# Kernel tuning notes

Measured on AMD Instinct MI355X. Metric: run time of the kernel, lower is better.

The kernel has to match this reference:

```python
import jax, jax.numpy as jnp
import numpy as np
from jax import lax

EPS = 1e-8
CAGE_SIZE = 1.4
DIST_THRESH = 0.4
CAGE_ITERS = 100
CAGE_STEP = 0.01


def _icosphere_div1():
    # icosahedron with one loop subdivision -> 42 verts, 80 faces, unit sphere
    t = (1.0 + 5.0 ** 0.5) / 2.0
    v = np.array([[-1, t, 0], [1, t, 0], [-1, -t, 0], [1, -t, 0],
                  [0, -1, t], [0, 1, t], [0, -1, -t], [0, 1, -t],
                  [t, 0, -1], [t, 0, 1], [-t, 0, -1], [-t, 0, 1]], dtype=np.float64)
    v /= np.linalg.norm(v, axis=1, keepdims=True)
    f = [[0, 11, 5], [0, 5, 1], [0, 1, 7], [0, 7, 10], [0, 10, 11],
         [1, 5, 9], [5, 11, 4], [11, 10, 2], [10, 7, 6], [7, 1, 8],
         [3, 9, 4], [3, 4, 2], [3, 2, 6], [3, 6, 8], [3, 8, 9],
         [4, 9, 5], [2, 4, 11], [6, 2, 10], [8, 6, 7], [9, 8, 1]]
    verts = list(v)
    cache = {}
    def mid(a, b):
        key = (min(a, b), max(a, b))
        if key not in cache:
            m = verts[a] + verts[b]
            verts.append(m / np.linalg.norm(m))
            cache[key] = len(verts) - 1
        return cache[key]
    nf = []
    for a, b, c in f:
        ab, bc, ca = mid(a, b), mid(b, c), mid(c, a)
        nf += [[a, ab, ca], [b, bc, ab], [c, ca, bc], [ab, bc, ca]]
    return np.stack(verts).astype(np.float32), np.array(nf, dtype=np.int32)


def _optimize_cage(cage, shape):
    # cage: (B,3,V), shape: (B,3,N). Pull cage toward origin until close to shape.
    def step(c, _):
        diff = c[:, :, :, None] - shape[:, :, None, :]          # (B,3,V,N)
        dist = jnp.sqrt(jnp.sum(diff * diff, axis=1))           # (B,V,N)
        min_d = jnp.min(dist, axis=2)                           # (B,V)
        upd = (min_d > DIST_THRESH).astype(c.dtype)
        return c + CAGE_STEP * (-c) * upd[:, None], None
    cage, _ = lax.scan(step, cage, None, length=CAGE_ITERS)
    return cage


def _mvc_weights(query, verts, faces):
    # 3D mean value coordinates (Ju et al. 2005).
    # query: (B,P,3), verts: (B,V,3), faces: (F,3) int -> weights (B,P,V)
    B, P, _ = query.shape
    V = verts.shape[1]
    F = faces.shape[0]
    u = verts[:, None] - query[:, :, None]                      # (B,P,V,3)
    d = jnp.linalg.norm(u, axis=-1)                             # (B,P,V)
    u = u / jnp.maximum(d, EPS)[..., None]
    uf = u[:, :, faces]                                         # (B,P,F,3,3)
    df = d[:, :, faces]                                         # (B,P,F,3)
    # edge lengths on unit sphere between opposite corner directions
    l = jnp.linalg.norm(jnp.roll(uf, -1, axis=3) - jnp.roll(uf, 1, axis=3), axis=-1)  # (B,P,F,3)
    theta = 2.0 * jnp.arcsin(jnp.clip(0.5 * l, 0.0, 1.0))
    h = 0.5 * jnp.sum(theta, axis=-1)                           # (B,P,F)
    sin_t = jnp.sin(theta)
    c = (2.0 * jnp.sin(h)[..., None] * jnp.sin(h[..., None] - theta)
         / jnp.maximum(jnp.roll(sin_t, -1, axis=-1) * jnp.roll(sin_t, 1, axis=-1), EPS)) - 1.0
    u0, u1, u2 = uf[..., 0, :], uf[..., 1, :], uf[..., 2, :]
    det = jnp.sum(u0 * jnp.cross(u1, u2), axis=-1)              # (B,P,F)
    s = jnp.sign(det)[..., None] * jnp.sqrt(jnp.clip(1.0 - c * c, 0.0, None))  # (B,P,F,3)
    valid = jnp.all(jnp.abs(s) > EPS, axis=-1)                  # coplanar-outside -> face contributes 0
    num = (theta - jnp.roll(c, -1, axis=-1) * jnp.roll(theta, 1, axis=-1)
           - jnp.roll(c, 1, axis=-1) * jnp.roll(theta, -1, axis=-1))
    den = df * jnp.roll(sin_t, -1, axis=-1) * jnp.roll(s, 1, axis=-1)
    den = jnp.where(jnp.abs(den) > EPS, den, jnp.where(den >= 0, EPS, -EPS))
    w = jnp.where(valid[..., None], num / den, 0.0)             # (B,P,F,3)
    W = jnp.zeros((B, P, V), dtype=query.dtype).at[:, :, faces.reshape(-1)].add(
        w.reshape(B, P, F * 3))
    sW = jnp.sum(W, axis=-1, keepdims=True)
    sW = jnp.where(jnp.abs(sW) > EPS, sW, EPS)
    return W / sW


def setup_inputs() -> dict:
    key = jax.random.key(0)
    ks = jax.random.split(key, 5)
    B, N, K = 4, 6144, 8
    v, f = _icosphere_div1()
    template_vertices = jnp.asarray(CAGE_SIZE * v.T[None])      # (1,3,42)
    return {
        "catModel": jax.random.normal(ks[0], (B, N, 3), dtype=jnp.float32),
        "catKeys": jax.random.normal(ks[1], (B, K, 3), dtype=jnp.float32),
        "catInflu": 0.1 * jax.random.normal(ks[2], (B, K, 42), dtype=jnp.float32),
        "insKeys": jax.random.normal(ks[3], (B, K, 3), dtype=jnp.float32),
        "insModel": jax.random.normal(ks[4], (B, N, 3), dtype=jnp.float32),
        "template_vertices": template_vertices,
        "template_faces": jnp.asarray(f),
    }


def reference(catModel, catKeys, catInflu, insKeys, insModel, template_vertices, template_faces):
    B = catModel.shape[0]
    cat_sh = jnp.swapaxes(catModel, 1, 2)                       # (B,3,N)
    cage = jnp.broadcast_to(template_vertices, (B,) + template_vertices.shape[1:])  # (B,3,42)
    cage = _optimize_cage(cage, cat_sh)
    # keypoint-driven cage offset via influence matrix
    kp_off = jnp.swapaxes(insKeys - catKeys, 1, 2)              # (B,3,8)
    cage_off = jnp.sum(kp_off[..., None] * catInflu[:, None], axis=2)  # (B,3,42)
    new_cage = cage + cage_off
    cage_v = jnp.swapaxes(cage, 1, 2)                           # (B,42,3)
    new_cage_v = jnp.swapaxes(new_cage, 1, 2)
    weights = _mvc_weights(catModel, cage_v, template_faces)    # (B,N,42)
    deformed = jnp.einsum('bnv,bvd->bnd', weights, new_cage_v)  # (B,N,3)
    # symmetric chamfer (squared L2, mean over points then batch, summed directions)
    d2 = jnp.sum((deformed[:, :, None] - insModel[:, None]) ** 2, axis=-1)  # (B,N,N)
    sim_loss = jnp.mean(jnp.min(d2, axis=2)) + jnp.mean(jnp.min(d2, axis=1))
    return (catModel, insModel, deformed, sim_loss)
```

## Files before the change

kernel.cpp:

```cpp
#include <hip/hip_runtime.h>
#include <hip/hip_bf16.h>
#include <math.h>

#define EPSF 1e-8f

static constexpr int FI[80][3] = {
  {0,12,14},{11,13,12},{5,14,13},{12,13,14},
  {0,14,16},{5,15,14},{1,16,15},{14,15,16},
  {0,16,18},{1,17,16},{7,18,17},{16,17,18},
  {0,18,20},{7,19,18},{10,20,19},{18,19,20},
  {0,20,12},{10,21,20},{11,12,21},{20,21,12},
  {1,15,23},{5,22,15},{9,23,22},{15,22,23},
  {5,13,25},{11,24,13},{4,25,24},{13,24,25},
  {11,21,27},{10,26,21},{2,27,26},{21,26,27},
  {10,19,29},{7,28,19},{6,29,28},{19,28,29},
  {7,17,31},{1,30,17},{8,31,30},{17,30,31},
  {3,32,34},{9,33,32},{4,34,33},{32,33,34},
  {3,34,36},{4,35,34},{2,36,35},{34,35,36},
  {3,36,38},{2,37,36},{6,38,37},{36,37,38},
  {3,38,40},{6,39,38},{8,40,39},{38,39,40},
  {3,40,32},{8,41,40},{9,32,41},{40,41,32},
  {4,33,25},{9,22,33},{5,25,22},{33,22,25},
  {2,35,27},{4,24,35},{11,27,24},{35,24,27},
  {6,37,29},{2,26,37},{10,29,26},{37,26,29},
  {8,39,31},{6,28,39},{7,31,28},{39,28,31},
  {9,41,23},{8,30,41},{1,23,30},{41,30,23}
};

__global__ __launch_bounds__(512) void k_cage(
    const float* __restrict__ catModel,
    const float* __restrict__ tv,
    const float* __restrict__ catKeys,
    const float* __restrict__ insKeys,
    const float* __restrict__ catInflu,
    float* __restrict__ cage,
    float* __restrict__ ncage)
{
  const int b = blockIdx.x / 42, v = blockIdx.x % 42;
  const int tid = threadIdx.x;
  const int lane = tid & 63, w = tid >> 6;
  const float c0x = tv[v], c0y = tv[42 + v], c0z = tv[84 + v];
  const float a = c0x*c0x + c0y*c0y + c0z*c0z;

  float pb2[12], pc[12];
  const float* P = catModel + (size_t)b * 6144 * 3;
  #pragma unroll
  for (int j = 0; j < 12; ++j) {
    int n = tid + j * 512;
    float px = P[n*3+0], py = P[n*3+1], pz = P[n*3+2];
    pb2[j] = -2.0f * (c0x*px + c0y*py + c0z*pz);
    pc[j]  = px*px + py*py + pz*pz;
  }

  __shared__ int mm[8];
  __shared__ float sfin;

  int tmin = 1000;
  float s = 1.0f;
  for (int t = 0; t < 100; ++t) {
    float ma = 1e30f, mb = 1e30f, mc = 1e30f, md = 1e30f;
    #pragma unroll
    for (int j = 0; j < 12; j += 4) {
      ma = fminf(ma, fmaf(fmaf(a, s, pb2[j+0]), s, pc[j+0]));
      mb = fminf(mb, fmaf(fmaf(a, s, pb2[j+1]), s, pc[j+1]));
      mc = fminf(mc, fmaf(fmaf(a, s, pb2[j+2]), s, pc[j+2]));
      md = fminf(md, fmaf(fmaf(a, s, pb2[j+3]), s, pc[j+3]));
    }
    float m = fminf(fminf(ma, mb), fminf(mc, md));
    if (m <= 0.16f && tmin == 1000) tmin = t;
    if (__all(tmin != 1000)) break;
    s *= 0.99f;
  }

  #pragma unroll
  for (int off = 32; off; off >>= 1)
    tmin = min(tmin, __shfl_xor(tmin, off, 64));
  if (lane == 0) mm[w] = tmin;
  __syncthreads();

  if (tid == 0) {
    int k = mm[0];
    #pragma unroll
    for (int i = 1; i < 8; ++i) k = min(k, mm[i]);
    if (k > 100) k = 100;
    float sf = 1.0f;
    for (int i = 0; i < k; ++i) sf *= 0.99f;
    sfin = sf;
  }
  __syncthreads();

  if (tid < 3) {
    const int d = tid;
    const float cg = sfin * tv[d*42 + v];
    float off = 0.0f;
    #pragma unroll
    for (int k = 0; k < 8; ++k)
      off += (insKeys[(b*8+k)*3 + d] - catKeys[(b*8+k)*3 + d]) * catInflu[(b*8+k)*42 + v];
    cage [(b*42 + v)*3 + d] = cg;
    ncage[(b*42 + v)*3 + d] = cg + off;
  }
}

__global__ __launch_bounds__(256) void k_mvc(
    const float* __restrict__ catModel,
    const float* __restrict__ cage,
    const float* __restrict__ ncage,
    float* __restrict__ outCat,
    float* __restrict__ outDef)
{
  const int b    = blockIdx.x / 384;
  const int pblk = blockIdx.x % 384;
  const int lane = threadIdx.x & 63;
  const int w    = threadIdx.x >> 6;
  const int pt   = lane & 15;
  const int sub  = lane >> 4;
  const int slice = w*4 + sub;
  const int p    = pblk * 16 + pt;

  __shared__ float cv[126], nv[126];
  __shared__ unsigned sF[80];
  __shared__ float red[4][4][16];
  if (threadIdx.x < 126) {
    cv[threadIdx.x] = cage [b*126 + threadIdx.x];
    nv[threadIdx.x] = ncage[b*126 + threadIdx.x];
  }
  if (threadIdx.x < 80) {
    sF[threadIdx.x] = (unsigned)FI[threadIdx.x][0]
                    | ((unsigned)FI[threadIdx.x][1] << 8)
                    | ((unsigned)FI[threadIdx.x][2] << 16);
  }
  __syncthreads();

  const float qx = catModel[((size_t)b*6144 + p)*3 + 0];
  const float qy = catModel[((size_t)b*6144 + p)*3 + 1];
  const float qz = catModel[((size_t)b*6144 + p)*3 + 2];

  if (w == 1 && sub == 0) {
    outCat[((size_t)b*6144 + p)*3 + 0] = qx;
    outCat[((size_t)b*6144 + p)*3 + 1] = qy;
    outCat[((size_t)b*6144 + p)*3 + 2] = qz;
  }

  float sW = 0.0f, dx = 0.0f, dy = 0.0f, dz = 0.0f;

  for (int ff = 0; ff < 5; ++ff) {
    const unsigned pk = sF[slice*5 + ff];
    const int i0 = pk & 255, i1 = (pk >> 8) & 255, i2 = pk >> 16;

    float e0x = cv[i0*3+0]-qx, e0y = cv[i0*3+1]-qy, e0z = cv[i0*3+2]-qz;
    float e1x = cv[i1*3+0]-qx, e1y = cv[i1*3+1]-qy, e1z = cv[i1*3+2]-qz;
    float e2x = cv[i2*3+0]-qx, e2y = cv[i2*3+1]-qy, e2z = cv[i2*3+2]-qz;
    float d0 = sqrtf(e0x*e0x + e0y*e0y + e0z*e0z);
    float d1 = sqrtf(e1x*e1x + e1y*e1y + e1z*e1z);
    float d2 = sqrtf(e2x*e2x + e2y*e2y + e2z*e2z);
    float r0 = 1.0f / fmaxf(d0, EPSF);
    float r1 = 1.0f / fmaxf(d1, EPSF);
    float r2 = 1.0f / fmaxf(d2, EPSF);
    float u0x = e0x*r0, u0y = e0y*r0, u0z = e0z*r0;
    float u1x = e1x*r1, u1y = e1y*r1, u1z = e1z*r1;
    float u2x = e2x*r2, u2y = e2y*r2, u2z = e2z*r2;

    float ax_ = u1x-u2x, ay_ = u1y-u2y, az_ = u1z-u2z;
    float bx_ = u2x-u0x, by_ = u2y-u0y, bz_ = u2z-u0z;
    float cx_ = u0x-u1x, cy_ = u0y-u1y, cz_ = u0z-u1z;
    float l0 = sqrtf(ax_*ax_ + ay_*ay_ + az_*az_);
    float l1 = sqrtf(bx_*bx_ + by_*by_ + bz_*bz_);
    float l2 = sqrtf(cx_*cx_ + cy_*cy_ + cz_*cz_);

    float s0 = fminf(0.5f*l0, 1.0f);
    float s1 = fminf(0.5f*l1, 1.0f);
    float s2 = fminf(0.5f*l2, 1.0f);
    float th0 = 2.0f*asinf(s0), th1 = 2.0f*asinf(s1), th2 = 2.0f*asinf(s2);
    float co0 = sqrtf(fmaxf(fmaf(-s0, s0, 1.0f), 0.0f));
    float co1 = sqrtf(fmaxf(fmaf(-s1, s1, 1.0f), 0.0f));
    float co2 = sqrtf(fmaxf(fmaf(-s2, s2, 1.0f), 0.0f));
    float st0 = 2.0f*s0*co0;
    float st1 = 2.0f*s1*co1;
    float st2 = 2.0f*s2*co2;

    float Sh = s0*co1*co2 + co0*s1*co2 + co0*co1*s2 - s0*s1*s2;
    float Ch = co0*co1*co2 - s0*s1*co2 - s0*co1*s2 - co0*s1*s2;
    float sh0 = Sh*fmaf(-2.0f*s0, s0, 1.0f) - Ch*st0;
    float sh1 = Sh*fmaf(-2.0f*s1, s1, 1.0f) - Ch*st1;
    float sh2 = Sh*fmaf(-2.0f*s2, s2, 1.0f) - Ch*st2;

    float c0 = 2.0f*Sh*sh0 / fmaxf(st1*st2, EPSF) - 1.0f;
    float c1 = 2.0f*Sh*sh1 / fmaxf(st2*st0, EPSF) - 1.0f;
    float c2 = 2.0f*Sh*sh2 / fmaxf(st0*st1, EPSF) - 1.0f;

    float det = u0x*(u1y*u2z - u1z*u2y)
              + u0y*(u1z*u2x - u1x*u2z)
              + u0z*(u1x*u2y - u1y*u2x);
    float sg = (det > 0.0f) ? 1.0f : ((det < 0.0f) ? -1.0f : 0.0f);
    float q0 = sg * sqrtf(fmaxf(fmaf(-c0, c0, 1.0f), 0.0f));
    float q1 = sg * sqrtf(fmaxf(fmaf(-c1, c1, 1.0f), 0.0f));
    float q2 = sg * sqrtf(fmaxf(fmaf(-c2, c2, 1.0f), 0.0f));
    bool valid = (fabsf(q0) > EPSF) && (fabsf(q1) > EPSF) && (fabsf(q2) > EPSF);

    float n0 = th0 - c1*th2 - c2*th1;
    float n1 = th1 - c2*th0 - c0*th2;
    float n2 = th2 - c0*th1 - c1*th0;
    float de0 = d0*st1*q2;
    float de1 = d1*st2*q0;
    float de2 = d2*st0*q1;
    de0 = (fabsf(de0) > EPSF) ? de0 : ((de0 >= 0.0f) ? EPSF : -EPSF);
    de1 = (fabsf(de1) > EPSF) ? de1 : ((de1 >= 0.0f) ? EPSF : -EPSF);
    de2 = (fabsf(de2) > EPSF) ? de2 : ((de2 >= 0.0f) ? EPSF : -EPSF);

    if (valid) {
      float w0 = n0/de0, w1 = n1/de1, w2 = n2/de2;
      sW += w0 + w1 + w2;
      dx = fmaf(w0, nv[i0*3+0], fmaf(w1, nv[i1*3+0], fmaf(w2, nv[i2*3+0], dx)));
      dy = fmaf(w0, nv[i0*3+1], fmaf(w1, nv[i1*3+1], fmaf(w2, nv[i2*3+1], dy)));
      dz = fmaf(w0, nv[i0*3+2], fmaf(w1, nv[i1*3+2], fmaf(w2, nv[i2*3+2], dz)));
    }
  }

  sW += __shfl_xor(sW, 16, 64); dx += __shfl_xor(dx, 16, 64);
  dy += __shfl_xor(dy, 16, 64); dz += __shfl_xor(dz, 16, 64);
  sW += __shfl_xor(sW, 32, 64); dx += __shfl_xor(dx, 32, 64);
  dy += __shfl_xor(dy, 32, 64); dz += __shfl_xor(dz, 32, 64);

  if (sub == 0) {
    red[w][0][pt] = sW; red[w][1][pt] = dx;
    red[w][2][pt] = dy; red[w][3][pt] = dz;
  }
  __syncthreads();

  if (w == 0 && sub == 0) {
    float S = red[0][0][pt] + red[1][0][pt] + red[2][0][pt] + red[3][0][pt];
    float X = red[0][1][pt] + red[1][1][pt] + red[2][1][pt] + red[3][1][pt];
    float Y = red[0][2][pt] + red[1][2][pt] + red[2][2][pt] + red[3][2][pt];
    float Z = red[0][3][pt] + red[1][3][pt] + red[2][3][pt] + red[3][3][pt];
    S = (fabsf(S) > EPSF) ? S : EPSF;
    float inv = 1.0f / S;
    outDef[((size_t)b*6144 + p)*3 + 0] = X * inv;
    outDef[((size_t)b*6144 + p)*3 + 1] = Y * inv;
    outDef[((size_t)b*6144 + p)*3 + 2] = Z * inv;
  }
}

__global__ __launch_bounds__(256) void k_chamfer(
    const float* __restrict__ def,
    const float* __restrict__ ins,
    float*       __restrict__ outIns,
    float*       __restrict__ partial,
    float*       __restrict__ loss)
{
  const int bx  = blockIdx.x;
  const int dir = (bx >= 384) ? 1 : 0;
  const int r   = bx - dir*384;
  const int b   = r / 96;
  const int rt  = (r % 96) / 24;
  const int cc  = r % 24;
  const int tid = threadIdx.x;

  if (bx == 0 && tid == 0) loss[0] = 0.0f;

  const float* R = (dir ? ins : def) + (size_t)b * 6144 * 3;
  const float* C = (dir ? def : ins) + (size_t)b * 6144 * 3;

  const int r0 = rt*1536 + tid;
  float rx[6], ry[6], rz[6];
  #pragma unroll
  for (int k = 0; k < 6; ++k) {
    int rr = r0 + k*256;
    rx[k] = R[rr*3+0]; ry[k] = R[rr*3+1]; rz[k] = R[rr*3+2];
  }

  if (dir == 1 && cc == 0) {
    #pragma unroll
    for (int k = 0; k < 6; ++k) {
      int rr = r0 + k*256;
      outIns[(size_t)(b*6144 + rr)*3+0] = rx[k];
      outIns[(size_t)(b*6144 + rr)*3+1] = ry[k];
      outIns[(size_t)(b*6144 + rr)*3+2] = rz[k];
    }
  }

  __shared__ float4 tile[256];
  {
    int c = cc*256 + tid;
    float cx = C[c*3+0], cy = C[c*3+1], cz = C[c*3+2];
    tile[tid] = make_float4(-2.0f*cx, -2.0f*cy, -2.0f*cz, cx*cx + cy*cy + cz*cz);
  }
  __syncthreads();

  float m[6];
  #pragma unroll
  for (int k = 0; k < 6; ++k) m[k] = 1e30f;

  #pragma unroll 8
  for (int j = 0; j < 256; ++j) {
    float4 q = tile[j];
    #pragma unroll
    for (int k = 0; k < 6; ++k)
      m[k] = fminf(m[k], fmaf(q.x, rx[k], fmaf(q.y, ry[k], fmaf(q.z, rz[k], q.w))));
  }

  float* po = partial + ((size_t)((dir*4 + b)*24 + cc)) * 6144;
  #pragma unroll
  for (int k = 0; k < 6; ++k) {
    int rr = r0 + k*256;
    po[rr] = m[k] + (rx[k]*rx[k] + ry[k]*ry[k] + rz[k]*rz[k]);
  }
}

__global__ __launch_bounds__(256) void k_loss(
    const float* __restrict__ partial,
    float* __restrict__ loss)
{
  const int base = blockIdx.x * 512 + threadIdx.x * 2;
  float s = 0.0f;
  #pragma unroll
  for (int g = base; g < base + 2; ++g) {
    const int db = g / 6144, row = g % 6144;
    const float* pp = partial + (size_t)db * 24 * 6144 + row;
    float v = 1e30f;
    #pragma unroll
    for (int c = 0; c < 24; ++c) v = fminf(v, pp[c * 6144]);
    s += v;
  }
  #pragma unroll
  for (int off = 32; off; off >>= 1) s += __shfl_xor(s, off, 64);
  __shared__ float red[4];
  if ((threadIdx.x & 63) == 0) red[threadIdx.x >> 6] = s;
  __syncthreads();
  if (threadIdx.x == 0)
    atomicAdd(loss, (red[0] + red[1] + red[2] + red[3]) * (1.0f / 24576.0f));
}

extern "C" void kernel_launch(void* const* d_in, const int* in_sizes, int n_in,
                              void* d_out, int out_size, void* d_ws, size_t ws_size,
                              hipStream_t stream) {
  const float* catModel = (const float*)d_in[0];
  const float* catKeys  = (const float*)d_in[1];
  const float* catInflu = (const float*)d_in[2];
  const float* insKeys  = (const float*)d_in[3];
  const float* insModel = (const float*)d_in[4];
  const float* tv       = (const float*)d_in[5];

  float* out = (float*)d_out;
  float* ws  = (float*)d_ws;
  float* cage    = ws;
  float* ncage   = ws + 512;
  float* partial = ws + 1024;

  k_cage<<<168, 512, 0, stream>>>(catModel, tv, catKeys, insKeys, catInflu, cage, ncage);
  k_mvc <<<1536, 256, 0, stream>>>(catModel, cage, ncage, out, out + 147456);
  k_chamfer<<<768, 256, 0, stream>>>(out + 147456, insModel, out + 73728, partial, out + 221184);
  k_loss<<<96, 256, 0, stream>>>(partial, out + 221184);
}
```

Measured before the change: 138.0 us.

## Fuse cage, MVC, chamfer and loss into one cooperative kernel with grid syncs

Replaces the four separate kernel launches with a single cooperative kernel of 512 blocks that runs each stage in turn, with grid.sync between stages, so launch gaps and inter-kernel drain are removed. Each block processes several MVC point tiles and up to two chamfer tiles. The cage stage now uses 256 threads per block, so each thread holds twice as many points, and only 168 of 512 blocks do work in that stage. If the cooperative launch fails, it falls back to the original four-kernel path. This adds grid-wide barrier cost, and the fused kernel's register pressure may limit occupancy.

```diff
diff --git a/kernel.cpp b/kernel.cpp
--- a/kernel.cpp
+++ b/kernel.cpp
@@ -1,6 +1,9 @@
 #include <hip/hip_runtime.h>
 #include <hip/hip_bf16.h>
+#include <hip/hip_cooperative_groups.h>
 #include <math.h>
+
+namespace cg = cooperative_groups;
 
 #define EPSF 1e-8f
 
@@ -27,122 +30,11 @@
   {9,41,23},{8,30,41},{1,23,30},{41,30,23}
 };
 
-__global__ __launch_bounds__(512) void k_cage(
-    const float* __restrict__ catModel,
-    const float* __restrict__ tv,
-    const float* __restrict__ catKeys,
-    const float* __restrict__ insKeys,
-    const float* __restrict__ catInflu,
-    float* __restrict__ cage,
-    float* __restrict__ ncage)
+__device__ __forceinline__ void mvc_slice(
+    const float* cv, const float* nv, const unsigned* sF,
+    int slice, float qx, float qy, float qz,
+    float& sW, float& dx, float& dy, float& dz)
 {
-  const int b = blockIdx.x / 42, v = blockIdx.x % 42;
-  const int tid = threadIdx.x;
-  const int lane = tid & 63, w = tid >> 6;
-  const float c0x = tv[v], c0y = tv[42 + v], c0z = tv[84 + v];
-  const float a = c0x*c0x + c0y*c0y + c0z*c0z;
-
-  float pb2[12], pc[12];
-  const float* P = catModel + (size_t)b * 6144 * 3;
-  #pragma unroll
-  for (int j = 0; j < 12; ++j) {
-    int n = tid + j * 512;
-    float px = P[n*3+0], py = P[n*3+1], pz = P[n*3+2];
-    pb2[j] = -2.0f * (c0x*px + c0y*py + c0z*pz);
-    pc[j]  = px*px + py*py + pz*pz;
-  }
-
-  __shared__ int mm[8];
-  __shared__ float sfin;
-
-  int tmin = 1000;
-  float s = 1.0f;
-  for (int t = 0; t < 100; ++t) {
-    float ma = 1e30f, mb = 1e30f, mc = 1e30f, md = 1e30f;
-    #pragma unroll
-    for (int j = 0; j < 12; j += 4) {
-      ma = fminf(ma, fmaf(fmaf(a, s, pb2[j+0]), s, pc[j+0]));
-      mb = fminf(mb, fmaf(fmaf(a, s, pb2[j+1]), s, pc[j+1]));
-      mc = fminf(mc, fmaf(fmaf(a, s, pb2[j+2]), s, pc[j+2]));
-      md = fminf(md, fmaf(fmaf(a, s, pb2[j+3]), s, pc[j+3]));
-    }
-    float m = fminf(fminf(ma, mb), fminf(mc, md));
-    if (m <= 0.16f && tmin == 1000) tmin = t;
-    if (__all(tmin != 1000)) break;
-    s *= 0.99f;
-  }
-
-  #pragma unroll
-  for (int off = 32; off; off >>= 1)
-    tmin = min(tmin, __shfl_xor(tmin, off, 64));
-  if (lane == 0) mm[w] = tmin;
-  __syncthreads();
-
-  if (tid == 0) {
-    int k = mm[0];
-    #pragma unroll
-    for (int i = 1; i < 8; ++i) k = min(k, mm[i]);
-    if (k > 100) k = 100;
-    float sf = 1.0f;
-    for (int i = 0; i < k; ++i) sf *= 0.99f;
-    sfin = sf;
-  }
-  __syncthreads();
-
-  if (tid < 3) {
-    const int d = tid;
-    const float cg = sfin * tv[d*42 + v];
-    float off = 0.0f;
-    #pragma unroll
-    for (int k = 0; k < 8; ++k)
-      off += (insKeys[(b*8+k)*3 + d] - catKeys[(b*8+k)*3 + d]) * catInflu[(b*8+k)*42 + v];
-    cage [(b*42 + v)*3 + d] = cg;
-    ncage[(b*42 + v)*3 + d] = cg + off;
-  }
-}
-
-__global__ __launch_bounds__(256) void k_mvc(
-    const float* __restrict__ catModel,
-    const float* __restrict__ cage,
-    const float* __restrict__ ncage,
-    float* __restrict__ outCat,
-    float* __restrict__ outDef)
-{
-  const int b    = blockIdx.x / 384;
-  const int pblk = blockIdx.x % 384;
-  const int lane = threadIdx.x & 63;
-  const int w    = threadIdx.x >> 6;
-  const int pt   = lane & 15;
-  const int sub  = lane >> 4;
-  const int slice = w*4 + sub;
-  const int p    = pblk * 16 + pt;
-
-  __shared__ float cv[126], nv[126];
-  __shared__ unsigned sF[80];
-  __shared__ float red[4][4][16];
-  if (threadIdx.x < 126) {
-    cv[threadIdx.x] = cage [b*126 + threadIdx.x];
-    nv[threadIdx.x] = ncage[b*126 + threadIdx.x];
-  }
-  if (threadIdx.x < 80) {
-    sF[threadIdx.x] = (unsigned)FI[threadIdx.x][0]
-                    | ((unsigned)FI[threadIdx.x][1] << 8)
-                    | ((unsigned)FI[threadIdx.x][2] << 16);
-  }
-  __syncthreads();
-
-  const float qx = catModel[((size_t)b*6144 + p)*3 + 0];
-  const float qy = catModel[((size_t)b*6144 + p)*3 + 1];
-  const float qz = catModel[((size_t)b*6144 + p)*3 + 2];
-
-  if (w == 1 && sub == 0) {
-    outCat[((size_t)b*6144 + p)*3 + 0] = qx;
-    outCat[((size_t)b*6144 + p)*3 + 1] = qy;
-    outCat[((size_t)b*6144 + p)*3 + 2] = qz;
-  }
-
-  float sW = 0.0f, dx = 0.0f, dy = 0.0f, dz = 0.0f;
-
   for (int ff = 0; ff < 5; ++ff) {
     const unsigned pk = sF[slice*5 + ff];
     const int i0 = pk & 255, i1 = (pk >> 8) & 255, i2 = pk >> 16;
@@ -215,6 +107,350 @@
       dz = fmaf(w0, nv[i0*3+2], fmaf(w1, nv[i1*3+2], fmaf(w2, nv[i2*3+2], dz)));
     }
   }
+}
+
+__global__ __launch_bounds__(256, 2) void k_fused(
+    const float* __restrict__ catModel, const float* __restrict__ catKeys,
+    const float* __restrict__ catInflu, const float* __restrict__ insKeys,
+    const float* __restrict__ insModel, const float* __restrict__ tv,
+    float* __restrict__ outCat, float* __restrict__ outIns,
+    float* __restrict__ outDef, float* __restrict__ loss,
+    float* __restrict__ cage, float* __restrict__ ncage,
+    float* __restrict__ partial)
+{
+  cg::grid_group grid = cg::this_grid();
+  const int bx  = blockIdx.x;
+  const int tid = threadIdx.x;
+  const int lane = tid & 63;
+  const int w    = tid >> 6;
+
+  __shared__ int   mm[4];
+  __shared__ float sfin;
+  __shared__ float cv[126], nv[126];
+  __shared__ unsigned sF[80];
+  __shared__ float red[4][4][16];
+  __shared__ float4 tile[256];
+  __shared__ float lred[4];
+
+  if (bx == 0 && tid == 0) loss[0] = 0.0f;
+  if (bx < 168) {
+    const int b = bx / 42, v = bx % 42;
+    const float c0x = tv[v], c0y = tv[42 + v], c0z = tv[84 + v];
+    const float a = c0x*c0x + c0y*c0y + c0z*c0z;
+
+    float pb2[24], pc[24];
+    const float* P = catModel + (size_t)b * 6144 * 3;
+    #pragma unroll
+    for (int j = 0; j < 24; ++j) {
+      int n = tid + j * 256;
+      float px = P[n*3+0], py = P[n*3+1], pz = P[n*3+2];
+      pb2[j] = -2.0f * (c0x*px + c0y*py + c0z*pz);
+      pc[j]  = px*px + py*py + pz*pz;
+    }
+
+    int tmin = 1000;
+    float s = 1.0f;
+    for (int t = 0; t < 100; ++t) {
+      float ma = 1e30f, mb = 1e30f, mc = 1e30f, md = 1e30f;
+      #pragma unroll
+      for (int j = 0; j < 24; j += 4) {
+        ma = fminf(ma, fmaf(fmaf(a, s, pb2[j+0]), s, pc[j+0]));
+        mb = fminf(mb, fmaf(fmaf(a, s, pb2[j+1]), s, pc[j+1]));
+        mc = fminf(mc, fmaf(fmaf(a, s, pb2[j+2]), s, pc[j+2]));
+        md = fminf(md, fmaf(fmaf(a, s, pb2[j+3]), s, pc[j+3]));
+      }
+      float m = fminf(fminf(ma, mb), fminf(mc, md));
+      if (m <= 0.16f && tmin == 1000) tmin = t;
+      if (__all(tmin != 1000)) break;
+      s *= 0.99f;
+    }
+
+    #pragma unroll
+    for (int off = 32; off; off >>= 1)
+      tmin = min(tmin, __shfl_xor(tmin, off, 64));
+    if (lane == 0) mm[w] = tmin;
+    __syncthreads();
+
+    if (tid == 0) {
+      int k = min(min(mm[0], mm[1]), min(mm[2], mm[3]));
+      if (k > 100) k = 100;
+      float sf = 1.0f;
+      for (int i = 0; i < k; ++i) sf *= 0.99f;
+      sfin = sf;
+    }
+    __syncthreads();
+
+    if (tid < 3) {
+      const int d = tid;
+      const float cg_ = sfin * tv[d*42 + v];
+      float off = 0.0f;
+      #pragma unroll
+      for (int k = 0; k < 8; ++k)
+        off += (insKeys[(b*8+k)*3 + d] - catKeys[(b*8+k)*3 + d]) * catInflu[(b*8+k)*42 + v];
+      cage [(b*42 + v)*3 + d] = cg_;
+      ncage[(b*42 + v)*3 + d] = cg_ + off;
+    }
+  }
+
+  __threadfence();
+  grid.sync();
+
+  {
+    const int job0 = bx * 3;
+    const int b = job0 / 384;
+    if (tid < 126) {
+      cv[tid] = cage [b*126 + tid];
+      nv[tid] = ncage[b*126 + tid];
+    }
+    if (tid < 80) {
+      sF[tid] = (unsigned)FI[tid][0] | ((unsigned)FI[tid][1] << 8)
+              | ((unsigned)FI[tid][2] << 16);
+    }
+    __syncthreads();
+
+    const int pt   = lane & 15;
+    const int sub  = lane >> 4;
+    const int slice = w*4 + sub;
+
+    for (int h = 0; h < 3; ++h) {
+      const int pblk = (job0 + h) % 384;
+      const int p    = pblk * 16 + pt;
+
+      const float qx = catModel[((size_t)b*6144 + p)*3 + 0];
+      const float qy = catModel[((size_t)b*6144 + p)*3 + 1];
+      const float qz = catModel[((size_t)b*6144 + p)*3 + 2];
+
+      if (w == 1 && sub == 0) {
+        outCat[((size_t)b*6144 + p)*3 + 0] = qx;
+        outCat[((size_t)b*6144 + p)*3 + 1] = qy;
+        outCat[((size_t)b*6144 + p)*3 + 2] = qz;
+      }
+
+      float sW = 0.0f, dx = 0.0f, dy = 0.0f, dz = 0.0f;
+      mvc_slice(cv, nv, sF, slice, qx, qy, qz, sW, dx, dy, dz);
+
+      sW += __shfl_xor(sW, 16, 64); dx += __shfl_xor(dx, 16, 64);
+      dy += __shfl_xor(dy, 16, 64); dz += __shfl_xor(dz, 16, 64);
+      sW += __shfl_xor(sW, 32, 64); dx += __shfl_xor(dx, 32, 64);
+      dy += __shfl_xor(dy, 32, 64); dz += __shfl_xor(dz, 32, 64);
+
+      if (sub == 0) {
+        red[w][0][pt] = sW; red[w][1][pt] = dx;
+        red[w][2][pt] = dy; red[w][3][pt] = dz;
+      }
+      __syncthreads();
+
+      if (w == 0 && sub == 0) {
+        float S = red[0][0][pt] + red[1][0][pt] + red[2][0][pt] + red[3][0][pt];
+        float X = red[0][1][pt] + red[1][1][pt] + red[2][1][pt] + red[3][1][pt];
+        float Y = red[0][2][pt] + red[1][2][pt] + red[2][2][pt] + red[3][2][pt];
+        float Z = red[0][3][pt] + red[1][3][pt] + red[2][3][pt] + red[3][3][pt];
+        S = (fabsf(S) > EPSF) ? S : EPSF;
+        float inv = 1.0f / S;
+        outDef[((size_t)b*6144 + p)*3 + 0] = X * inv;
+        outDef[((size_t)b*6144 + p)*3 + 1] = Y * inv;
+        outDef[((size_t)b*6144 + p)*3 + 2] = Z * inv;
+      }
+      __syncthreads();
+    }
+  }
+
+  __threadfence();
+  grid.sync();
+
+  for (int jj = 0; jj < 2; ++jj) {
+    const int jb = bx + jj*512;
+    if (jb >= 768) break;
+    const int dir = (jb >= 384) ? 1 : 0;
+    const int r   = jb - dir*384;
+    const int b   = r / 96;
+    const int rt  = (r % 96) / 24;
+    const int cc  = r % 24;
+
+    const float* R = (dir ? insModel : outDef) + (size_t)b * 6144 * 3;
+    const float* C = (dir ? outDef : insModel) + (size_t)b * 6144 * 3;
+
+    const int r0 = rt*1536 + tid;
+    float rx[6], ry[6], rz[6];
+    #pragma unroll
+    for (int k = 0; k < 6; ++k) {
+      int rr = r0 + k*256;
+      rx[k] = R[rr*3+0]; ry[k] = R[rr*3+1]; rz[k] = R[rr*3+2];
+    }
+
+    if (dir == 1 && cc == 0) {
+      #pragma unroll
+      for (int k = 0; k < 6; ++k) {
+        int rr = r0 + k*256;
+        outIns[(size_t)(b*6144 + rr)*3+0] = rx[k];
+        outIns[(size_t)(b*6144 + rr)*3+1] = ry[k];
+        outIns[(size_t)(b*6144 + rr)*3+2] = rz[k];
+      }
+    }
+
+    __syncthreads();
+    {
+      int c = cc*256 + tid;
+      float cx = C[c*3+0], cy = C[c*3+1], cz = C[c*3+2];
+      tile[tid] = make_float4(-2.0f*cx, -2.0f*cy, -2.0f*cz, cx*cx + cy*cy + cz*cz);
+    }
+    __syncthreads();
+
+    float m[6];
+    #pragma unroll
+    for (int k = 0; k < 6; ++k) m[k] = 1e30f;
+
+    #pragma unroll 8
+    for (int j = 0; j < 256; ++j) {
+      float4 q = tile[j];
+      #pragma unroll
+      for (int k = 0; k < 6; ++k)
+        m[k] = fminf(m[k], fmaf(q.x, rx[k], fmaf(q.y, ry[k], fmaf(q.z, rz[k], q.w))));
+    }
+
+    float* po = partial + ((size_t)((dir*4 + b)*24 + cc)) * 6144;
+    #pragma unroll
+    for (int k = 0; k < 6; ++k) {
+      int rr = r0 + k*256;
+      po[rr] = m[k] + (rx[k]*rx[k] + ry[k]*ry[k] + rz[k]*rz[k]);
+    }
+  }
+
+  __threadfence();
+  grid.sync();
+
+  if (bx < 96) {
+    const int base = bx * 512 + tid * 2;
+    float s = 0.0f;
+    #pragma unroll
+    for (int g = base; g < base + 2; ++g) {
+      const int db = g / 6144, row = g % 6144;
+      const float* pp = partial + (size_t)db * 24 * 6144 + row;
+      float v = 1e30f;
+      #pragma unroll
+      for (int c = 0; c < 24; ++c) v = fminf(v, pp[c * 6144]);
+      s += v;
+    }
+    #pragma unroll
+    for (int off = 32; off; off >>= 1) s += __shfl_xor(s, off, 64);
+    if (lane == 0) lred[w] = s;
+    __syncthreads();
+    if (tid == 0)
+      atomicAdd(loss, (lred[0] + lred[1] + lred[2] + lred[3]) * (1.0f / 24576.0f));
+  }
+}
+
+__global__ __launch_bounds__(512) void k_cage(
+    const float* __restrict__ catModel, const float* __restrict__ tv,
+    const float* __restrict__ catKeys, const float* __restrict__ insKeys,
+    const float* __restrict__ catInflu,
+    float* __restrict__ cage, float* __restrict__ ncage)
+{
+  const int b = blockIdx.x / 42, v = blockIdx.x % 42;
+  const int tid = threadIdx.x;
+  const int lane = tid & 63, w = tid >> 6;
+  const float c0x = tv[v], c0y = tv[42 + v], c0z = tv[84 + v];
+  const float a = c0x*c0x + c0y*c0y + c0z*c0z;
+
+  float pb2[12], pc[12];
+  const float* P = catModel + (size_t)b * 6144 * 3;
+  #pragma unroll
+  for (int j = 0; j < 12; ++j) {
+    int n = tid + j * 512;
+    float px = P[n*3+0], py = P[n*3+1], pz = P[n*3+2];
+    pb2[j] = -2.0f * (c0x*px + c0y*py + c0z*pz);
+    pc[j]  = px*px + py*py + pz*pz;
+  }
+
+  __shared__ int mm[8];
+  __shared__ float sfin;
+
+  int tmin = 1000;
+  float s = 1.0f;
+  for (int t = 0; t < 100; ++t) {
+    float ma = 1e30f, mb = 1e30f, mc = 1e30f, md = 1e30f;
+    #pragma unroll
+    for (int j = 0; j < 12; j += 4) {
+      ma = fminf(ma, fmaf(fmaf(a, s, pb2[j+0]), s, pc[j+0]));
+      mb = fminf(mb, fmaf(fmaf(a, s, pb2[j+1]), s, pc[j+1]));
+      mc = fminf(mc, fmaf(fmaf(a, s, pb2[j+2]), s, pc[j+2]));
+      md = fminf(md, fmaf(fmaf(a, s, pb2[j+3]), s, pc[j+3]));
+    }
+    float m = fminf(fminf(ma, mb), fminf(mc, md));
+    if (m <= 0.16f && tmin == 1000) tmin = t;
+    if (__all(tmin != 1000)) break;
+    s *= 0.99f;
+  }
+
+  #pragma unroll
+  for (int off = 32; off; off >>= 1)
+    tmin = min(tmin, __shfl_xor(tmin, off, 64));
+  if (lane == 0) mm[w] = tmin;
+  __syncthreads();
+
+  if (tid == 0) {
+    int k = mm[0];
+    #pragma unroll
+    for (int i = 1; i < 8; ++i) k = min(k, mm[i]);
+    if (k > 100) k = 100;
+    float sf = 1.0f;
+    for (int i = 0; i < k; ++i) sf *= 0.99f;
+    sfin = sf;
+  }
+  __syncthreads();
+
+  if (tid < 3) {
+    const int d = tid;
+    const float cg_ = sfin * tv[d*42 + v];
+    float off = 0.0f;
+    #pragma unroll
+    for (int k = 0; k < 8; ++k)
+      off += (insKeys[(b*8+k)*3 + d] - catKeys[(b*8+k)*3 + d]) * catInflu[(b*8+k)*42 + v];
+    cage [(b*42 + v)*3 + d] = cg_;
+    ncage[(b*42 + v)*3 + d] = cg_ + off;
+  }
+}
+
+__global__ __launch_bounds__(256) void k_mvc(
+    const float* __restrict__ catModel, const float* __restrict__ cage,
+    const float* __restrict__ ncage,
+    float* __restrict__ outCat, float* __restrict__ outDef)
+{
+  const int b    = blockIdx.x / 384;
+  const int pblk = blockIdx.x % 384;
+  const int lane = threadIdx.x & 63;
+  const int w    = threadIdx.x >> 6;
+  const int pt   = lane & 15;
+  const int sub  = lane >> 4;
+  const int slice = w*4 + sub;
+  const int p    = pblk * 16 + pt;
+
+  __shared__ float cv[126], nv[126];
+  __shared__ unsigned sF[80];
+  __shared__ float red[4][4][16];
+  if (threadIdx.x < 126) {
+    cv[threadIdx.x] = cage [b*126 + threadIdx.x];
+    nv[threadIdx.x] = ncage[b*126 + threadIdx.x];
+  }
+  if (threadIdx.x < 80) {
+    sF[threadIdx.x] = (unsigned)FI[threadIdx.x][0]
+                    | ((unsigned)FI[threadIdx.x][1] << 8)
+                    | ((unsigned)FI[threadIdx.x][2] << 16);
+  }
+  __syncthreads();
+
+  const float qx = catModel[((size_t)b*6144 + p)*3 + 0];
+  const float qy = catModel[((size_t)b*6144 + p)*3 + 1];
+  const float qz = catModel[((size_t)b*6144 + p)*3 + 2];
+
+  if (w == 1 && sub == 0) {
+    outCat[((size_t)b*6144 + p)*3 + 0] = qx;
+    outCat[((size_t)b*6144 + p)*3 + 1] = qy;
+    outCat[((size_t)b*6144 + p)*3 + 2] = qz;
+  }
+
+  float sW = 0.0f, dx = 0.0f, dy = 0.0f, dz = 0.0f;
+  mvc_slice(cv, nv, sF, slice, qx, qy, qz, sW, dx, dy, dz);
 
   sW += __shfl_xor(sW, 16, 64); dx += __shfl_xor(dx, 16, 64);
   dy += __shfl_xor(dy, 16, 64); dz += __shfl_xor(dz, 16, 64);
@@ -241,11 +477,9 @@
 }
 
 __global__ __launch_bounds__(256) void k_chamfer(
-    const float* __restrict__ def,
-    const float* __restrict__ ins,
-    float*       __restrict__ outIns,
-    float*       __restrict__ partial,
-    float*       __restrict__ loss)
+    const float* __restrict__ def, const float* __restrict__ ins,
+    float* __restrict__ outIns, float* __restrict__ partial,
+    float* __restrict__ loss)
 {
   const int bx  = blockIdx.x;
   const int dir = (bx >= 384) ? 1 : 0;
@@ -307,8 +541,7 @@
 }
 
 __global__ __launch_bounds__(256) void k_loss(
-    const float* __restrict__ partial,
-    float* __restrict__ loss)
+    const float* __restrict__ partial, float* __restrict__ loss)
 {
   const int base = blockIdx.x * 512 + threadIdx.x * 2;
   float s = 0.0f;
@@ -346,8 +579,23 @@
   float* ncage   = ws + 512;
   float* partial = ws + 1024;
 
-  k_cage<<<168, 512, 0, stream>>>(catModel, tv, catKeys, insKeys, catInflu, cage, ncage);
-  k_mvc <<<1536, 256, 0, stream>>>(catModel, cage, ncage, out, out + 147456);
-  k_chamfer<<<768, 256, 0, stream>>>(out + 147456, insModel, out + 73728, partial, out + 221184);
-  k_loss<<<96, 256, 0, stream>>>(partial, out + 221184);
+  float* outCat = out;
+  float* outIns = out + 73728;
+  float* outDef = out + 147456;
+  float* loss   = out + 221184;
+
+  void* args[] = { (void*)&catModel, (void*)&catKeys, (void*)&catInflu,
+                   (void*)&insKeys, (void*)&insModel, (void*)&tv,
+                   (void*)&outCat, (void*)&outIns, (void*)&outDef,
+                   (void*)&loss, (void*)&cage, (void*)&ncage, (void*)&partial };
+
+  hipError_t e = hipLaunchCooperativeKernel((void*)k_fused, dim3(512), dim3(256),
+                                            args, 0, stream);
+  if (e != hipSuccess) {
+    (void)hipGetLastError();
+    k_cage<<<168, 512, 0, stream>>>(catModel, tv, catKeys, insKeys, catInflu, cage, ncage);
+    k_mvc <<<1536, 256, 0, stream>>>(catModel, cage, ncage, outCat, outDef);
+    k_chamfer<<<768, 256, 0, stream>>>(outDef, insModel, outIns, partial, loss);
+    k_loss<<<96, 256, 0, stream>>>(partial, loss);
+  }
 }
```

New measurement: 435.5 us. 3.16x slower.
